# Kernel optimization log

Hardware: AMD Instinct MI355X
Metric: run time of the kernel (lower is better)

Reference implementation:

```python
import jax, jax.numpy as jnp
import numpy as np

L = 24
D = 2048
NUM_BLOCKS = 8
EPS = 1e-6
B, T = 2, 1024


def _block_layout(num_layers, num_blocks):
    base = num_layers // num_blocks
    rem = num_layers % num_blocks
    sizes = [base] * num_blocks
    if rem:
        sizes[-1] += rem
    starts = list(np.cumsum([0] + sizes[:-1]))
    return sizes, starts


def _rmsnorm(x, weight, eps=EPS):
    # x: (..., d)
    var = jnp.mean(x * x, axis=-1, keepdims=True)
    return x * jax.lax.rsqrt(var + eps) * weight


def setup_inputs() -> dict:
    key = jax.random.key(0)
    k1, k2, k3 = jax.random.split(key, 3)
    layer_outputs = jax.random.normal(k1, (L, B, T, D), dtype=jnp.float32)
    embedding = jax.random.normal(k2, (B, T, D), dtype=jnp.float32)
    queries = jax.random.normal(k3, (L, D), dtype=jnp.float32) * 0.02
    key_norm_weight = jnp.ones((D,), dtype=jnp.float32)
    return {
        "layer_outputs": layer_outputs,
        "embedding": embedding,
        "queries": queries,
        "key_norm_weight": key_norm_weight,
    }


def reference(layer_outputs, embedding, queries, key_norm_weight):
    """Faithful port of BlockAttnRes.compute_all_inputs.

    layer_outputs: (L, B, T, d)  -- f_l(h_l) for each layer
    embedding:     (B, T, d)     -- b_0
    queries:       (L, d)        -- zero-init pseudo-queries (randn here)
    key_norm_weight: (d,)        -- RMSNorm scale
    Returns (L, B, T, d): AttnRes input h_l for each layer.
    """
    num_layers = layer_outputs.shape[0]
    sizes, starts = _block_layout(num_layers, NUM_BLOCKS)

    block_reprs = [embedding]
    partial = None
    inputs = []
    block_n = 0
    for l in range(num_layers):  # fixed structural loop over layers
        # advance block index
        while l >= starts[block_n] + sizes[block_n]:
            block_n += 1
        i = l - starts[block_n]
        sources = list(block_reprs)
        if i > 0 and partial is not None:
            sources.append(partial)
        v_stack = jnp.stack(sources, axis=2)            # (B, T, n, d)
        k_stack = _rmsnorm(v_stack, key_norm_weight)    # (B, T, n, d)
        scores = jnp.einsum("btnd,d->btn", k_stack, queries[l])
        alpha = jax.nn.softmax(scores, axis=-1)         # (B, T, n)
        h = jnp.einsum("btn,btnd->btd", alpha, v_stack)
        inputs.append(h)
        f_l = layer_outputs[l]
        partial = f_l if partial is None else partial + f_l
        if i + 1 >= sizes[block_n]:
            block_reprs.append(partial)
            partial = None
    return jnp.stack(inputs, axis=0)  # (L, B, T, d)
```

## Files before the change

kernel.cpp:

```cpp
#include <hip/hip_runtime.h>
#include <hip/hip_bf16.h>

constexpr int LAYERS = 24;
constexpr int DIM    = 2048;
constexpr int NBLK   = 8;
constexpr float EPSV = 1e-6f;
constexpr int TPB    = 512;
constexpr int EPT    = 4;
constexpr int NSLOT  = 147;
constexpr int ASLOT  = 49;
constexpr int RSTR   = NSLOT + 2;

typedef float vf4 __attribute__((ext_vector_type(4)));

__device__ constexpr int OFF_TAB[24] =
    {0,1,4,7,10,14,18,22,27,32,37,43,49,55,62,69,76,84,92,100,109,118,127,137};
__device__ constexpr int SSQS[7] = {9,21,36,54,75,99,126};

__device__ __forceinline__ unsigned pk2(float a, float b) {
    __hip_bfloat162 h2(__float2bfloat16(a), __float2bfloat16(b));
    union { __hip_bfloat162 h; unsigned u; } c; c.h = h2; return c.u;
}
__device__ __forceinline__ float upk(unsigned p, int hi) {
    union { unsigned u; float f; } c;
    c.u = hi ? (p & 0xffff0000u) : (p << 16);
    return c.f;
}

template<int CTRL>
__device__ __forceinline__ float dpp_add(float x) {
    int y = __builtin_amdgcn_update_dpp(0, __float_as_int(x), CTRL, 0xF, 0xF, true);
    return x + __int_as_float(y);
}
__device__ __forceinline__ float grp16_sum(float x) {
    x = dpp_add<0xB1>(x);
    x = dpp_add<0x4E>(x);
    x = dpp_add<0x141>(x);
    x = dpp_add<0x140>(x);
    return x;
}

__global__ void prep_qw_kernel(const float* __restrict__ q,
                               const float* __restrict__ w,
                               float* __restrict__ qw, int n) {
    int idx = blockIdx.x * blockDim.x + threadIdx.x;
    if (idx < n) qw[idx] = q[idx] * w[idx & (DIM - 1)];
}

template<bool PREMUL>
__global__ void __launch_bounds__(TPB, 4)
block_attn_res_kernel(const float* __restrict__ lo,
                      const float* __restrict__ emb,
                      const float* __restrict__ q1,
                      const float* __restrict__ wgt,
                      float* __restrict__ out,
                      int bt_total)
{
    const int bt   = blockIdx.x;
    const int tid  = threadIdx.x;
    const int lane = tid & 63;
    const int wid  = tid >> 6;
    const int grp  = (wid << 2) | (lane >> 4);
    const int c0   = tid * 4;

    __shared__ float red[32][RSTR];
    __shared__ float redJ[NSLOT + 1];
    __shared__ float ab[LAYERS][12];

    const float invD = 1.f / (float)DIM;
    const size_t lstride = (size_t)bt_total * DIM;
    const float* lop = lo + (size_t)bt * DIM + c0;

    auto wred = [&](float x, int slot) {
        x = grp16_sum(x);
        if ((lane & 15) == 0) red[grp][slot] = x;
    };

    float wv[EPT];
    if (!PREMUL) {
        vf4 w0 = *reinterpret_cast<const vf4*>(wgt + c0);
        wv[0]=w0.x; wv[1]=w0.y; wv[2]=w0.z; wv[3]=w0.w;
    }

    float e[EPT];
    {
        vf4 v0 = __builtin_nontemporal_load(
            reinterpret_cast<const vf4*>(emb + (size_t)bt * DIM + c0));
        e[0]=v0.x; e[1]=v0.y; e[2]=v0.z; e[3]=v0.w;
    }

    unsigned pp[16][EPT/2];
    unsigned Spk[NBLK-1][EPT/2];
    float part[EPT];

    auto emit = [&](int l) {
        const int m = l / 3;
        const int i = l - 3 * m;
        float h[EPT];
        {
            const float a0 = ab[l][0];
            #pragma unroll
            for (int j = 0; j < EPT; ++j) h[j] = a0 * e[j];
        }
        #pragma unroll
        for (int s = 0; s < NBLK - 1; ++s) {
            if (s < m) {
                const float a = ab[l][1 + s];
                h[0] += a * upk(Spk[s][0],0);
                h[1] += a * upk(Spk[s][0],1);
                h[2] += a * upk(Spk[s][1],0);
                h[3] += a * upk(Spk[s][1],1);
            }
        }
        if (i > 0) {
            const float a = ab[l][1 + m];
            const int si = 2 * m + (i - 1);
            h[0] += a * upk(pp[si][0],0);
            h[1] += a * upk(pp[si][0],1);
            h[2] += a * upk(pp[si][1],0);
            h[3] += a * upk(pp[si][1],1);
        }
        vf4 w0; w0.x=h[0]; w0.y=h[1]; w0.z=h[2]; w0.w=h[3];
        *reinterpret_cast<vf4*>(out + ((size_t)l * bt_total + bt) * DIM + c0) = w0;
    };

    float fb[4][EPT], qb[2][EPT];
    auto p1_body = [&](int l) {
        const int m   = l / 3;
        const int i   = l - 3 * m;
        const int off = OFF_TAB[l];
        const int pf  = l & 3;
        const int pq  = l & 1;

        float qwv[EPT];
        #pragma unroll
        for (int j = 0; j < EPT; ++j)
            qwv[j] = PREMUL ? qb[pq][j] : qb[pq][j] * wv[j];
        float fC[EPT];
        if (l < LAYERS - 1) {
            #pragma unroll
            for (int j = 0; j < EPT; ++j) fC[j] = fb[pf][j];
        }

        if (l + 4 <= LAYERS - 2) {
            vf4 u0 = __builtin_nontemporal_load(
                reinterpret_cast<const vf4*>(lop + (size_t)(l + 4) * lstride));
            fb[pf][0]=u0.x; fb[pf][1]=u0.y; fb[pf][2]=u0.z; fb[pf][3]=u0.w;
        }
        if (l + 2 <= LAYERS - 1) {
            vf4 v0 = *reinterpret_cast<const vf4*>(q1 + (size_t)(l + 2) * DIM + c0);
            qb[pq][0]=v0.x; qb[pq][1]=v0.y; qb[pq][2]=v0.z; qb[pq][3]=v0.w;
        }

        {
            float dv = e[0]*qwv[0] + e[1]*qwv[1] + e[2]*qwv[2] + e[3]*qwv[3];
            wred(dv, off);
        }
        #pragma unroll
        for (int s = 0; s < NBLK - 1; ++s) {
            if (s < m) {
                float dv;
                if (s == m - 1 && i == 0) {
                    dv = part[0]*qwv[0] + part[1]*qwv[1]
                       + part[2]*qwv[2] + part[3]*qwv[3];
                } else {
                    dv = upk(Spk[s][0],0)*qwv[0] + upk(Spk[s][0],1)*qwv[1]
                       + upk(Spk[s][1],0)*qwv[2] + upk(Spk[s][1],1)*qwv[3];
                }
                wred(dv, off + 1 + s);
            }
        }
        if (i > 0) {
            float dv = part[0]*qwv[0] + part[1]*qwv[1]
                     + part[2]*qwv[2] + part[3]*qwv[3];
            float sq = part[0]*part[0] + part[1]*part[1]
                     + part[2]*part[2] + part[3]*part[3];
            wred(dv, off + m + 1);
            wred(sq, off + m + 2);
            const int si = 2 * m + (i - 1);
            pp[si][0] = pk2(part[0], part[1]);
            pp[si][1] = pk2(part[2], part[3]);
        } else {
            float sq = part[0]*part[0] + part[1]*part[1]
                     + part[2]*part[2] + part[3]*part[3];
            wred(sq, off + m + 1);
        }

        if (l < LAYERS - 1) {
            if (i == 0) {
                #pragma unroll
                for (int j = 0; j < EPT; ++j) part[j] = fC[j];
            } else {
                #pragma unroll
                for (int j = 0; j < EPT; ++j) part[j] += fC[j];
            }
            if (i == 2 && m < NBLK - 1) {
                Spk[m][0] = pk2(part[0], part[1]);
                Spk[m][1] = pk2(part[2], part[3]);
            }
        }
    };

    auto softmax_l = [&](int l) {
        const int m = l / 3;
        const int i = l - 3 * m;
        const int off = OFF_TAB[l];
        const float ssqe = redJ[0];
        float sce = redJ[off] * rsqrtf(ssqe * invD + EPSV);
        float mx = sce;
        float scS[NBLK - 1];
        #pragma unroll
        for (int s = 0; s < NBLK - 1; ++s) {
            if (s < m) {
                scS[s] = redJ[off + 1 + s] * rsqrtf(redJ[SSQS[s]] * invD + EPSV);
                mx = fmaxf(mx, scS[s]);
            }
        }
        float scp = 0.f;
        if (i > 0) {
            scp = redJ[off + m + 1] * rsqrtf(redJ[off + m + 2] * invD + EPSV);
            mx = fmaxf(mx, scp);
        }
        float ee = __expf(sce - mx), den = ee;
        float es[NBLK - 1];
        #pragma unroll
        for (int s = 0; s < NBLK - 1; ++s) {
            es[s] = (s < m) ? __expf(scS[s] - mx) : 0.f;
            den += es[s];
        }
        float ep = 0.f;
        if (i > 0) { ep = __expf(scp - mx); den += ep; }
        const float inv = 1.f / den;
        ab[l][0] = ee * inv;
        #pragma unroll
        for (int s = 0; s < NBLK - 1; ++s)
            if (s < m) ab[l][1 + s] = es[s] * inv;
        if (i > 0) ab[l][1 + m] = ep * inv;
    };

    {
        vf4 u0 = __builtin_nontemporal_load(reinterpret_cast<const vf4*>(lop));
        part[0]=u0.x; part[1]=u0.y; part[2]=u0.z; part[3]=u0.w;

        vf4 w0; w0.x=e[0]; w0.y=e[1]; w0.z=e[2]; w0.w=e[3];
        *reinterpret_cast<vf4*>(out + (size_t)bt * DIM + c0) = w0;

        float sq = e[0]*e[0] + e[1]*e[1] + e[2]*e[2] + e[3]*e[3];
        wred(sq, 0);
    }
    {
        #pragma unroll
        for (int k = 1; k <= 4; ++k) {
            vf4 u = __builtin_nontemporal_load(
                reinterpret_cast<const vf4*>(lop + (size_t)k * lstride));
            fb[k & 3][0]=u.x; fb[k & 3][1]=u.y; fb[k & 3][2]=u.z; fb[k & 3][3]=u.w;
        }
        vf4 q;
        q = *reinterpret_cast<const vf4*>(q1 + (size_t)1 * DIM + c0);
        qb[1][0]=q.x; qb[1][1]=q.y; qb[1][2]=q.z; qb[1][3]=q.w;
        q = *reinterpret_cast<const vf4*>(q1 + (size_t)2 * DIM + c0);
        qb[0][0]=q.x; qb[0][1]=q.y; qb[0][2]=q.z; qb[0][3]=q.w;
    }
    #pragma unroll
    for (int l = 1; l <= 11; ++l) p1_body(l);

    __syncthreads();
    if (tid < ASLOT) {
        float s = 0.f;
        #pragma unroll
        for (int g = 0; g < 32; ++g) s += red[g][tid];
        redJ[tid] = s;
    }
    __syncthreads();
    if (tid >= 1 && tid <= 11) softmax_l(tid);
    __syncthreads();

    #pragma unroll
    for (int l = 12; l < LAYERS; ++l) {
        p1_body(l);
        if (l <= 22) emit(l - 11);
    }

    __syncthreads();
    if (tid < NSLOT - ASLOT) {
        const int slot = ASLOT + tid;
        float s = 0.f;
        #pragma unroll
        for (int g = 0; g < 32; ++g) s += red[g][slot];
        redJ[slot] = s;
    }
    __syncthreads();
    if (tid >= 12 && tid < LAYERS) softmax_l(tid);
    __syncthreads();

    #pragma unroll
    for (int l = 12; l < LAYERS; ++l) emit(l);
}

extern "C" void kernel_launch(void* const* d_in, const int* in_sizes, int n_in,
                              void* d_out, int out_size, void* d_ws, size_t ws_size,
                              hipStream_t stream) {
    const float* lo  = (const float*)d_in[0];
    const float* emb = (const float*)d_in[1];
    const float* qry = (const float*)d_in[2];
    const float* wgt = (const float*)d_in[3];
    float* outp = (float*)d_out;

    const int bt_total = in_sizes[1] / DIM;
    const int nq = in_sizes[2];

    if (ws_size >= (size_t)nq * sizeof(float)) {
        float* qwbuf = (float*)d_ws;
        prep_qw_kernel<<<(nq + 255) / 256, 256, 0, stream>>>(qry, wgt, qwbuf, nq);
        block_attn_res_kernel<true><<<bt_total, TPB, 0, stream>>>(
            lo, emb, qwbuf, nullptr, outp, bt_total);
    } else {
        block_attn_res_kernel<false><<<bt_total, TPB, 0, stream>>>(
            lo, emb, qry, wgt, outp, bt_total);
    }
}
```

Baseline: 179.1 us.

## Drop query premultiply kernel and split score/emit pipeline into three phases

Removes the separate prep kernel that multiplied queries by the norm weight, folding the multiply into the main kernel so only one launch runs. Restructures the score-reduction/softmax/emit schedule from two phases (layers 1-11, 12-23) to three phases (1-7, 8-15, 16-23). Output writes for earlier layers can then be interleaved with score computation of later layers, leaving a shorter tail of emits at the end. The cost is one extra pair of block-wide barriers and a few extra multiplies per layer.

```diff
diff --git a/kernel.cpp b/kernel.cpp
--- a/kernel.cpp
+++ b/kernel.cpp
@@ -8,7 +8,6 @@
 constexpr int TPB    = 512;
 constexpr int EPT    = 4;
 constexpr int NSLOT  = 147;
-constexpr int ASLOT  = 49;
 constexpr int RSTR   = NSLOT + 2;
 
 typedef float vf4 __attribute__((ext_vector_type(4)));
@@ -40,18 +39,10 @@
     return x;
 }
 
-__global__ void prep_qw_kernel(const float* __restrict__ q,
-                               const float* __restrict__ w,
-                               float* __restrict__ qw, int n) {
-    int idx = blockIdx.x * blockDim.x + threadIdx.x;
-    if (idx < n) qw[idx] = q[idx] * w[idx & (DIM - 1)];
-}
-
-template<bool PREMUL>
 __global__ void __launch_bounds__(TPB, 4)
 block_attn_res_kernel(const float* __restrict__ lo,
                       const float* __restrict__ emb,
-                      const float* __restrict__ q1,
+                      const float* __restrict__ qry,
                       const float* __restrict__ wgt,
                       float* __restrict__ out,
                       int bt_total)
@@ -77,7 +68,7 @@
     };
 
     float wv[EPT];
-    if (!PREMUL) {
+    {
         vf4 w0 = *reinterpret_cast<const vf4*>(wgt + c0);
         wv[0]=w0.x; wv[1]=w0.y; wv[2]=w0.z; wv[3]=w0.w;
     }
@@ -134,8 +125,7 @@
 
         float qwv[EPT];
         #pragma unroll
-        for (int j = 0; j < EPT; ++j)
-            qwv[j] = PREMUL ? qb[pq][j] : qb[pq][j] * wv[j];
+        for (int j = 0; j < EPT; ++j) qwv[j] = qb[pq][j] * wv[j];
         float fC[EPT];
         if (l < LAYERS - 1) {
             #pragma unroll
@@ -148,7 +138,7 @@
             fb[pf][0]=u0.x; fb[pf][1]=u0.y; fb[pf][2]=u0.z; fb[pf][3]=u0.w;
         }
         if (l + 2 <= LAYERS - 1) {
-            vf4 v0 = *reinterpret_cast<const vf4*>(q1 + (size_t)(l + 2) * DIM + c0);
+            vf4 v0 = *reinterpret_cast<const vf4*>(qry + (size_t)(l + 2) * DIM + c0);
             qb[pq][0]=v0.x; qb[pq][1]=v0.y; qb[pq][2]=v0.z; qb[pq][3]=v0.w;
         }
 
@@ -238,6 +228,16 @@
         if (i > 0) ab[l][1 + m] = ep * inv;
     };
 
+    auto join = [&](int slo, int shi) {
+        if (tid < shi - slo) {
+            const int slot = slo + tid;
+            float s = 0.f;
+            #pragma unroll
+            for (int g = 0; g < 32; ++g) s += red[g][slot];
+            redJ[slot] = s;
+        }
+    };
+
     {
         vf4 u0 = __builtin_nontemporal_load(reinterpret_cast<const vf4*>(lop));
         part[0]=u0.x; part[1]=u0.y; part[2]=u0.z; part[3]=u0.w;
@@ -256,45 +256,46 @@
             fb[k & 3][0]=u.x; fb[k & 3][1]=u.y; fb[k & 3][2]=u.z; fb[k & 3][3]=u.w;
         }
         vf4 q;
-        q = *reinterpret_cast<const vf4*>(q1 + (size_t)1 * DIM + c0);
+        q = *reinterpret_cast<const vf4*>(qry + (size_t)1 * DIM + c0);
         qb[1][0]=q.x; qb[1][1]=q.y; qb[1][2]=q.z; qb[1][3]=q.w;
-        q = *reinterpret_cast<const vf4*>(q1 + (size_t)2 * DIM + c0);
+        q = *reinterpret_cast<const vf4*>(qry + (size_t)2 * DIM + c0);
         qb[0][0]=q.x; qb[0][1]=q.y; qb[0][2]=q.z; qb[0][3]=q.w;
     }
     #pragma unroll
-    for (int l = 1; l <= 11; ++l) p1_body(l);
-
-    __syncthreads();
-    if (tid < ASLOT) {
-        float s = 0.f;
-        #pragma unroll
-        for (int g = 0; g < 32; ++g) s += red[g][tid];
-        redJ[tid] = s;
-    }
-    __syncthreads();
-    if (tid >= 1 && tid <= 11) softmax_l(tid);
+    for (int l = 1; l <= 7; ++l) p1_body(l);
+
+    __syncthreads();
+    join(0, 27);
+    __syncthreads();
+    if (tid >= 1 && tid <= 7) softmax_l(tid);
     __syncthreads();
 
     #pragma unroll
-    for (int l = 12; l < LAYERS; ++l) {
+    for (int l = 8; l <= 15; ++l) {
         p1_body(l);
-        if (l <= 22) emit(l - 11);
-    }
-
-    __syncthreads();
-    if (tid < NSLOT - ASLOT) {
-        const int slot = ASLOT + tid;
-        float s = 0.f;
-        #pragma unroll
-        for (int g = 0; g < 32; ++g) s += red[g][slot];
-        redJ[slot] = s;
-    }
-    __syncthreads();
-    if (tid >= 12 && tid < LAYERS) softmax_l(tid);
+        if (l <= 14) emit(l - 7);
+    }
+
+    __syncthreads();
+    join(27, 76);
+    __syncthreads();
+    if (tid >= 8 && tid <= 15) softmax_l(tid);
     __syncthreads();
 
     #pragma unroll
-    for (int l = 12; l < LAYERS; ++l) emit(l);
+    for (int l = 16; l <= 23; ++l) {
+        p1_body(l);
+        emit(l - 8);
+    }
+
+    __syncthreads();
+    join(76, 147);
+    __syncthreads();
+    if (tid >= 16 && tid <= 23) softmax_l(tid);
+    __syncthreads();
+
+    #pragma unroll
+    for (int l = 16; l <= 23; ++l) emit(l);
 }
 
 extern "C" void kernel_launch(void* const* d_in, const int* in_sizes, int n_in,
@@ -307,15 +308,7 @@
     float* outp = (float*)d_out;
 
     const int bt_total = in_sizes[1] / DIM;
-    const int nq = in_sizes[2];
-
-    if (ws_size >= (size_t)nq * sizeof(float)) {
-        float* qwbuf = (float*)d_ws;
-        prep_qw_kernel<<<(nq + 255) / 256, 256, 0, stream>>>(qry, wgt, qwbuf, nq);
-        block_attn_res_kernel<true><<<bt_total, TPB, 0, stream>>>(
-            lo, emb, qwbuf, nullptr, outp, bt_total);
-    } else {
-        block_attn_res_kernel<false><<<bt_total, TPB, 0, stream>>>(
-            lo, emb, qry, wgt, outp, bt_total);
-    }
-}
+
+    block_attn_res_kernel<<<bt_total, TPB, 0, stream>>>(
+        lo, emb, qry, wgt, outp, bt_total);
+}
```

Result: no change. 179.1 us (+0.0%).
